# Performance work log

Hardware: AMD Instinct MI355X
Metric: run time of the kernel (lower is better)

## Reference

```python
import jax, jax.numpy as jnp
import numpy as np

C = 256

def setup_inputs() -> dict:
    key = jax.random.key(0)
    ks = jax.random.split(key, 7)
    s = 1.0 / np.sqrt(C)
    x = jax.random.normal(ks[0], (4, C, 64, 64), dtype=jnp.float32)
    Wq = jax.random.uniform(ks[1], (C, C), jnp.float32, -s, s)
    bq = jax.random.uniform(ks[2], (C,), jnp.float32, -s, s)
    Wk = jax.random.uniform(ks[3], (C, C), jnp.float32, -s, s)
    bk = jax.random.uniform(ks[4], (C,), jnp.float32, -s, s)
    Wv = jax.random.uniform(ks[5], (C, C), jnp.float32, -s, s)
    bv = jax.random.uniform(ks[6], (C,), jnp.float32, -s, s)
    return {"x": x, "Wq": Wq, "bq": bq, "Wk": Wk, "bk": bk, "Wv": Wv, "bv": bv}

def reference(x, Wq, bq, Wk, bk, Wv, bv):
    B, Cc, H, W = x.shape
    N = H * W
    xf = x.reshape(B, Cc, N)                      # (B, C, N)
    # 1x1 conv == channel linear: out[b,o,n] = sum_c W[o,c] x[b,c,n] + b[o]
    q = jnp.einsum('oc,bcn->bno', Wq, xf) + bq    # (B, N, C)  proj_query^T
    k = jnp.einsum('oc,bcn->bon', Wk, xf) + bk[None, :, None]  # (B, C, N)
    v = jnp.einsum('oc,bcn->bon', Wv, xf) + bv[None, :, None]  # (B, C, N)
    energy = jnp.einsum('bnc,bcm->bnm', q, k)     # (B, N, N)
    attention = jax.nn.softmax(energy, axis=-1)
    # out = V @ attention^T : out[b,c,n] = sum_m v[b,c,m] * attention[b,n,m]
    out = jnp.einsum('bcm,bnm->bcn', v, attention)
    return out.reshape(B, Cc, H, W)
```

## Files before the change

kernel.cpp:

```cpp
#include <hip/hip_runtime.h>
#include <math.h>

#define BB 4
#define CC 256
#define NN 4096

using half8 = __attribute__((ext_vector_type(8))) _Float16;
using f32x4 = __attribute__((ext_vector_type(4))) float;

__device__ __forceinline__ unsigned short f2h(float f) {
  _Float16 h = (_Float16)f;
  return __builtin_bit_cast(unsigned short, h);
}
__device__ __forceinline__ float h2f(unsigned short u) {
  return (float)__builtin_bit_cast(_Float16, u);
}

#define ASYNC16(g, l)                                                        \
  __builtin_amdgcn_global_load_lds(                                          \
      (const __attribute__((address_space(1))) unsigned int*)(g),            \
      (__attribute__((address_space(3))) unsigned int*)(l), 16, 0, 0)

__device__ __forceinline__ int row512_off(int r, int chunk) {
  return r * 256 + (((chunk & 24) | ((chunk ^ r) & 7)) << 3);
}
__device__ __forceinline__ int vt_off(int r, int chunk) {
  return r * 64 + (((chunk ^ r) & 7) << 3);
}

__global__ __launch_bounds__(256) void k_wcast(const float* __restrict__ Wq,
    const float* __restrict__ Wk, const float* __restrict__ Wv,
    unsigned short* __restrict__ Wt) {
  int id = blockIdx.x * 256 + threadIdx.x;
  int pos8 = id & 7, o = (id >> 3) & 255, ks = (id >> 11) & 3, p3 = id >> 13;
  const float* W = p3 == 0 ? Wq : (p3 == 1 ? Wk : Wv);
  int c = ks * 64 + ((pos8 ^ o) & 7) * 8;
  const float* src = W + (size_t)o * CC + c;
  float4 a = *(const float4*)(src);
  float4 b4 = *(const float4*)(src + 4);
  union { unsigned short u[8]; uint4 v4; } pk;
  pk.u[0] = f2h(a.x);  pk.u[1] = f2h(a.y);  pk.u[2] = f2h(a.z);  pk.u[3] = f2h(a.w);
  pk.u[4] = f2h(b4.x); pk.u[5] = f2h(b4.y); pk.u[6] = f2h(b4.z); pk.u[7] = f2h(b4.w);
  *(uint4*)(Wt + (size_t)id * 8) = pk.v4;
}

__global__ __launch_bounds__(512) void k_proj(const float* __restrict__ x,
    const unsigned short* __restrict__ Wt,
    const float* __restrict__ bq, const float* __restrict__ bk,
    const float* __restrict__ bv,
    unsigned short* __restrict__ Q, unsigned short* __restrict__ K,
    unsigned short* __restrict__ V) {
  __shared__ __align__(16) char ps[110848];
  float* xf = (float*)ps;
  unsigned short* xa = (unsigned short*)(ps + 8448);
  unsigned short* wh = (unsigned short*)(ps + 12544);
  int b = blockIdx.y, n0 = blockIdx.x * 32;
  int t = threadIdx.x, w = t >> 6, lane = t & 63, l15 = lane & 15, quad = lane >> 4;

  f32x4 z = {0.f, 0.f, 0.f, 0.f};
  f32x4 acc[3][2][2];
#pragma unroll
  for (int p3 = 0; p3 < 3; ++p3)
#pragma unroll
    for (int ct = 0; ct < 2; ++ct)
#pragma unroll
      for (int mt = 0; mt < 2; ++mt) acc[p3][ct][mt] = z;

  for (int ks = 0; ks < 4; ++ks) {
    if (ks) __syncthreads();
#pragma unroll
    for (int p3 = 0; p3 < 3; ++p3) {
      const char* wb = (const char*)(Wt + (size_t)(p3 * 4 + ks) * 16384);
#pragma unroll
      for (int p = 0; p < 4; ++p) {
        int c = p * 512 + t;
        ASYNC16(wb + c * 16, &wh[p3 * 16384 + (p * 512 + (w << 6)) * 8]);
      }
    }
    {
      int c = t >> 3, nl = (t & 7) * 4;
      float4 v = *(const float4*)(x + ((size_t)b * CC + ks * 64 + c) * NN + n0 + nl);
      float* d = xf + c * 33 + nl;
      d[0] = v.x; d[1] = v.y; d[2] = v.z; d[3] = v.w;
    }
    __syncthreads();
    {
      int n = t >> 4, cb = (t & 15) * 4;
      union { unsigned short u[4]; ushort4 v4; } tmp;
#pragma unroll
      for (int i = 0; i < 4; ++i) tmp.u[i] = f2h(xf[(cb + i) * 33 + n]);
      int ch = cb >> 3;
      *(ushort4*)&xa[n * 64 + (((ch ^ n) & 7) << 3) + (cb & 7)] = tmp.v4;
    }
    __syncthreads();
#pragma unroll
    for (int kc = 0; kc < 2; ++kc) {
      half8 af[2];
#pragma unroll
      for (int mt = 0; mt < 2; ++mt)
        af[mt] = *(const half8*)&xa[vt_off(mt * 16 + l15, kc * 4 + quad)];
#pragma unroll
      for (int p3 = 0; p3 < 3; ++p3)
#pragma unroll
        for (int ct = 0; ct < 2; ++ct) {
          half8 bf = *(const half8*)&wh[p3 * 16384 + vt_off(w * 32 + ct * 16 + l15, kc * 4 + quad)];
#pragma unroll
          for (int mt = 0; mt < 2; ++mt)
            acc[p3][ct][mt] = __builtin_amdgcn_mfma_f32_16x16x32_f16(af[mt], bf, acc[p3][ct][mt], 0, 0, 0);
        }
    }
  }
#pragma unroll
  for (int p3 = 0; p3 < 3; ++p3) {
    const float* bias = p3 == 0 ? bq : (p3 == 1 ? bk : bv);
#pragma unroll
    for (int ct = 0; ct < 2; ++ct) {
      float bv_ = bias[w * 32 + ct * 16 + l15];
#pragma unroll
      for (int mt = 0; mt < 2; ++mt)
#pragma unroll
        for (int r = 0; r < 4; ++r) acc[p3][ct][mt][r] += bv_;
    }
  }
#pragma unroll
  for (int p3 = 0; p3 < 2; ++p3) {
    __syncthreads();
    unsigned short* qo = (unsigned short*)ps;
#pragma unroll
    for (int ct = 0; ct < 2; ++ct)
#pragma unroll
      for (int mt = 0; mt < 2; ++mt)
#pragma unroll
        for (int r = 0; r < 4; ++r)
          qo[(mt * 16 + quad * 4 + r) * 264 + w * 32 + ct * 16 + l15] = f2h(acc[p3][ct][mt][r]);
    __syncthreads();
    unsigned short* outp = (p3 == 0 ? Q : K) + ((size_t)b * NN + n0) * CC;
#pragma unroll
    for (int p = 0; p < 2; ++p) {
      int f = p * 8192 + t * 16;
      int n = f >> 9, off = f & 511;
      *(uint4*)((char*)outp + (size_t)n * 512 + off) =
        *(const uint4*)((const char*)&qo[n * 264] + off);
    }
  }
  {
    __syncthreads();
    unsigned short* vo = (unsigned short*)ps;
#pragma unroll
    for (int ct = 0; ct < 2; ++ct)
#pragma unroll
      for (int mt = 0; mt < 2; ++mt)
#pragma unroll
        for (int r = 0; r < 4; ++r)
          vo[(w * 32 + ct * 16 + l15) * 36 + mt * 16 + quad * 4 + r] = f2h(acc[2][ct][mt][r]);
    __syncthreads();
#pragma unroll
    for (int p = 0; p < 2; ++p) {
      int id = p * 512 + t;
      int o = id >> 2, off = (id & 3) * 16;
      *(uint4*)((char*)(V + ((size_t)b * CC + o) * NN + n0) + off) =
        *(const uint4*)((const char*)&vo[o * 36] + off);
    }
  }
}

__global__ __launch_bounds__(512) void k_flash(const unsigned short* __restrict__ Q,
    const unsigned short* __restrict__ K, const unsigned short* __restrict__ V,
    float* __restrict__ out, unsigned short* __restrict__ opart,
    float* __restrict__ ml, int n_splits) {
  __shared__ unsigned short ktA[16384], ktB[16384];
  __shared__ unsigned short vt[16384];
  __shared__ unsigned short pt[8192];
  __shared__ float al[128], ll[128];
  int b = blockIdx.y, q0 = blockIdx.x * 128, split = blockIdx.z;
  int nper = 64 / n_splits;
  int t = threadIdx.x, w = t >> 6, lane = t & 63, l15 = lane & 15, quad = lane >> 4;
  int g = w >> 1, h = w & 1;

  half8 qf[8];
  const unsigned short* qrow = Q + ((size_t)b * NN + q0 + w * 16 + l15) * CC;
#pragma unroll
  for (int k = 0; k < 8; ++k) qf[k] = *(const half8*)(qrow + k * 32 + quad * 8);

  f32x4 z = {0.f, 0.f, 0.f, 0.f};
  f32x4 o_acc[2][8];
#pragma unroll
  for (int mt = 0; mt < 2; ++mt)
#pragma unroll
    for (int i = 0; i < 8; ++i) o_acc[mt][i] = z;
  float m_i[4], lp_[4];
#pragma unroll
  for (int r = 0; r < 4; ++r) { m_i[r] = -INFINITY; lp_[r] = 0.f; }

  int it_beg = split * nper, it_end = it_beg + nper;

  auto dma_k = [&](int it, unsigned short* dst) {
    const char* kb = (const char*)(K + ((size_t)b * NN + it * 64) * CC);
#pragma unroll
    for (int p = 0; p < 4; ++p) {
      int c = p * 512 + t;
      int r = c >> 5, lo = c & 31;
      int ch = (lo & 24) | ((lo ^ r) & 7);
      ASYNC16(kb + r * 512 + ch * 16, &dst[(p * 512 + (w << 6)) * 8]);
    }
  };
  auto dma_v = [&](int it) {
    const char* vb = (const char*)(V + (size_t)b * CC * NN + it * 64);
#pragma unroll
    for (int p = 0; p < 4; ++p) {
      int c = p * 512 + t;
      int r = c >> 3;
      int ch = (c ^ r) & 7;
      ASYNC16(vb + (size_t)r * 8192 + ch * 16, &vt[(p * 512 + (w << 6)) * 8]);
    }
  };

  auto body = [&](const unsigned short* cur, unsigned short* nxt, int it) {
    if (it + 1 < it_end) dma_k(it + 1, nxt);
    dma_v(it);

    f32x4 sa[4];
#pragma unroll
    for (int j = 0; j < 4; ++j) sa[j] = z;
#pragma unroll
    for (int kk = 0; kk < 8; ++kk) {
#pragma unroll
      for (int j = 0; j < 4; ++j) {
        half8 bf = *(const half8*)&cur[row512_off(j * 16 + l15, kk * 4 + quad)];
        sa[j] = __builtin_amdgcn_mfma_f32_16x16x32_f16(qf[kk], bf, sa[j], 0, 0, 0);
      }
    }
    float mt4[4];
#pragma unroll
    for (int r = 0; r < 4; ++r)
      mt4[r] = fmaxf(fmaxf(sa[0][r], sa[1][r]), fmaxf(sa[2][r], sa[3][r]));
#pragma unroll
    for (int off = 1; off < 16; off <<= 1)
#pragma unroll
      for (int r = 0; r < 4; ++r)
        mt4[r] = fmaxf(mt4[r], __shfl_xor(mt4[r], off, 64));
    float alpha[4];
#pragma unroll
    for (int r = 0; r < 4; ++r) {
      float mn = fmaxf(m_i[r], mt4[r]);
      alpha[r] = __expf(m_i[r] - mn);
      m_i[r] = mn;
    }
#pragma unroll
    for (int r = 0; r < 4; ++r) {
      float ls = 0.f;
#pragma unroll
      for (int j = 0; j < 4; ++j) {
        float p = __expf(sa[j][r] - m_i[r]);
        sa[j][r] = p;
        ls += p;
      }
      lp_[r] = lp_[r] * alpha[r] + ls;
    }
    if (l15 == 0) {
#pragma unroll
      for (int r = 0; r < 4; ++r) al[w * 16 + quad * 4 + r] = alpha[r];
    }
#pragma unroll
    for (int j = 0; j < 4; ++j)
#pragma unroll
      for (int r = 0; r < 4; ++r) {
        int row = w * 16 + quad * 4 + r;
        int ch = 2 * j + (l15 >> 3);
        pt[row * 64 + (((ch ^ row) & 7) << 3) + (l15 & 7)] = f2h(sa[j][r]);
      }
    __syncthreads();

    float a_al[2][4];
#pragma unroll
    for (int mt = 0; mt < 2; ++mt)
#pragma unroll
      for (int r = 0; r < 4; ++r)
        a_al[mt][r] = al[g * 32 + mt * 16 + quad * 4 + r];
#pragma unroll
    for (int mt = 0; mt < 2; ++mt)
#pragma unroll
      for (int ct = 0; ct < 8; ++ct)
#pragma unroll
        for (int r = 0; r < 4; ++r) o_acc[mt][ct][r] *= a_al[mt][r];
#pragma unroll
    for (int ks2 = 0; ks2 < 2; ++ks2) {
      half8 af[2];
#pragma unroll
      for (int mt = 0; mt < 2; ++mt) {
        int row_p = g * 32 + mt * 16 + l15;
        af[mt] = *(const half8*)&pt[row_p * 64 + ((((ks2 * 4 + quad) ^ row_p) & 7) << 3)];
      }
#pragma unroll
      for (int ct = 0; ct < 8; ++ct) {
        half8 bf = *(const half8*)&vt[vt_off(h * 128 + ct * 16 + l15, ks2 * 4 + quad)];
#pragma unroll
        for (int mt = 0; mt < 2; ++mt)
          o_acc[mt][ct] = __builtin_amdgcn_mfma_f32_16x16x32_f16(af[mt], bf, o_acc[mt][ct], 0, 0, 0);
      }
    }
    __syncthreads();
  };

  dma_k(it_beg, ktA);
  __syncthreads();
  for (int it = it_beg; it < it_end; it += 2) {
    body(ktA, ktB, it);
    body(ktB, ktA, it + 1);
  }

#pragma unroll
  for (int off = 1; off < 16; off <<= 1)
#pragma unroll
    for (int r = 0; r < 4; ++r)
      lp_[r] += __shfl_xor(lp_[r], off, 64);
  if (l15 == 0) {
#pragma unroll
    for (int r = 0; r < 4; ++r) ll[w * 16 + quad * 4 + r] = lp_[r];
  }
  if (n_splits != 1 && l15 == 0) {
    size_t qi = (size_t)q0 + w * 16 + quad * 4;
    float* mp = ml + ((size_t)(split * 2 + 0) * BB + b) * NN + qi;
    float* lq = ml + ((size_t)(split * 2 + 1) * BB + b) * NN + qi;
#pragma unroll
    for (int r = 0; r < 4; ++r) { mp[r] = m_i[r]; lq[r] = lp_[r]; }
  }
  __syncthreads();
  float sc[2][4];
#pragma unroll
  for (int mt = 0; mt < 2; ++mt)
#pragma unroll
    for (int r = 0; r < 4; ++r) {
      float lv = ll[g * 32 + mt * 16 + quad * 4 + r];
      sc[mt][r] = (n_splits == 1) ? 1.f / lv : 1.f;
    }

  float* od = (float*)ktA;
  float* obf = out + (size_t)b * CC * NN + q0;
  unsigned short* obh = opart + ((size_t)split * BB + b) * CC * NN + q0;
#pragma unroll
  for (int pp = 0; pp < 8; ++pp) {
    __syncthreads();
    if (h == (pp >> 2)) {
#pragma unroll
      for (int cp = 0; cp < 2; ++cp) {
        int ct = (pp & 3) * 2 + cp;
#pragma unroll
        for (int mt = 0; mt < 2; ++mt)
#pragma unroll
          for (int r = 0; r < 4; ++r)
            od[(cp * 16 + l15) * 132 + g * 32 + mt * 16 + quad * 4 + r] =
                o_acc[mt][ct][r] * sc[mt][r];
      }
    }
    __syncthreads();
    if (n_splits == 1) {
#pragma unroll
      for (int p2 = 0; p2 < 2; ++p2) {
        int row = p2 * 16 + (t >> 5);
        *(float4*)(obf + (size_t)(pp * 32 + row) * NN + (t & 31) * 4) =
          *(const float4*)&od[row * 132 + (t & 31) * 4];
      }
    } else {
      int row = t >> 4, q8 = (t & 15) * 8;
      union { unsigned short u[8]; uint4 v4; } tmp;
#pragma unroll
      for (int i2 = 0; i2 < 8; ++i2) tmp.u[i2] = f2h(od[row * 132 + q8 + i2]);
      *(uint4*)(obh + (size_t)(pp * 32 + row) * NN + q8) = tmp.v4;
    }
  }
}

__global__ __launch_bounds__(256) void k_merge(const unsigned short* __restrict__ opart,
    const float* __restrict__ ml, float* __restrict__ out) {
  size_t i = ((size_t)blockIdx.x * 256 + threadIdx.x) * 4;
  int n = (int)(i & (NN - 1));
  int b = (int)(i >> 20);
  float4 m1 = *(const float4*)(ml + ((size_t)(0 * BB) + b) * NN + n);
  float4 l1 = *(const float4*)(ml + ((size_t)(1 * BB) + b) * NN + n);
  float4 m2 = *(const float4*)(ml + ((size_t)(2 * BB) + b) * NN + n);
  float4 l2 = *(const float4*)(ml + ((size_t)(3 * BB) + b) * NN + n);
  ushort4 o1 = *(const ushort4*)(opart + i);
  ushort4 o2 = *(const ushort4*)(opart + (size_t)BB * CC * NN + i);
  float4 res;
#define MRG(f, comp) { \
    float M = fmaxf(m1.f, m2.f); \
    float e1 = __expf(m1.f - M), e2 = __expf(m2.f - M); \
    res.f = (e1 * h2f(o1.comp) + e2 * h2f(o2.comp)) / (e1 * l1.f + e2 * l2.f); }
  MRG(x, x) MRG(y, y) MRG(z, z) MRG(w, w)
#undef MRG
  *(float4*)(out + i) = res;
}

extern "C" void kernel_launch(void* const* d_in, const int* in_sizes, int n_in,
                              void* d_out, int out_size, void* d_ws, size_t ws_size,
                              hipStream_t stream) {
  const float* x  = (const float*)d_in[0];
  const float* Wq = (const float*)d_in[1];
  const float* bq = (const float*)d_in[2];
  const float* Wk = (const float*)d_in[3];
  const float* bk = (const float*)d_in[4];
  const float* Wv = (const float*)d_in[5];
  const float* bv = (const float*)d_in[6];
  float* out = (float*)d_out;
  char* ws = (char*)d_ws;
  const size_t MB = 1024 * 1024;
  unsigned short* Qb = (unsigned short*)(ws);
  unsigned short* Kb = (unsigned short*)(ws + 8 * MB);
  unsigned short* Vb = (unsigned short*)(ws + 16 * MB);
  unsigned short* Op = (unsigned short*)(ws + 24 * MB);
  float*          Ml = (float*)(ws + 40 * MB);

  int ns = (ws_size >= 41 * MB) ? 2 : 1;
  unsigned short* Wt = (unsigned short*)(ns == 2 ? ws + 40 * MB + 256 * 1024
                                                 : ws + 24 * MB);

  k_wcast<<<dim3(96), 256, 0, stream>>>(Wq, Wk, Wv, Wt);
  k_proj<<<dim3(128, 4), 512, 0, stream>>>(x, Wt, bq, bk, bv, Qb, Kb, Vb);

  k_flash<<<dim3(32, 4, ns), 512, 0, stream>>>(Qb, Kb, Vb, out, Op, Ml, ns);
  if (ns == 2) k_merge<<<dim3(4096), 256, 0, stream>>>(Op, Ml, out);
}
```

Baseline: 212.0 us.

## Halve flash KV tile to 32, raise occupancy, add 4-way split merge

```diff
diff --git a/kernel.cpp b/kernel.cpp
--- a/kernel.cpp
+++ b/kernel.cpp
@@ -4,6 +4,7 @@
 #define BB 4
 #define CC 256
 #define NN 4096
+#define KV 32
 
 using half8 = __attribute__((ext_vector_type(8))) _Float16;
 using f32x4 = __attribute__((ext_vector_type(4))) float;
@@ -23,6 +24,9 @@
 
 __device__ __forceinline__ int row512_off(int r, int chunk) {
   return r * 256 + (((chunk & 24) | ((chunk ^ r) & 7)) << 3);
+}
+__device__ __forceinline__ int tile32_off(int r, int q) {
+  return (r >> 1) * 64 + (((((r & 1) << 2) | q) ^ ((r >> 1) & 7)) & 7) * 8;
 }
 __device__ __forceinline__ int vt_off(int r, int chunk) {
   return r * 64 + (((chunk ^ r) & 7) << 3);
@@ -164,16 +168,19 @@
   }
 }
 
-__global__ __launch_bounds__(512) void k_flash(const unsigned short* __restrict__ Q,
+__global__ __launch_bounds__(512, 4) void k_flash(const unsigned short* __restrict__ Q,
     const unsigned short* __restrict__ K, const unsigned short* __restrict__ V,
     float* __restrict__ out, unsigned short* __restrict__ opart,
     float* __restrict__ ml, int n_splits) {
-  __shared__ unsigned short ktA[16384], ktB[16384];
-  __shared__ unsigned short vt[16384];
-  __shared__ unsigned short pt[8192];
-  __shared__ float al[128], ll[128];
+  __shared__ __align__(16) char sm[58368];
+  unsigned short* kt0 = (unsigned short*)sm;
+  unsigned short* kt1 = (unsigned short*)(sm + 16384);
+  unsigned short* vt  = (unsigned short*)(sm + 32768);
+  unsigned short* pt  = (unsigned short*)(sm + 49152);
+  float* al = (float*)(sm + 57344);
+  float* ll = (float*)(sm + 57856);
   int b = blockIdx.y, q0 = blockIdx.x * 128, split = blockIdx.z;
-  int nper = 64 / n_splits;
+  int nt = (NN / KV) / n_splits;
   int t = threadIdx.x, w = t >> 6, lane = t & 63, l15 = lane & 15, quad = lane >> 4;
   int g = w >> 1, h = w & 1;
 
@@ -192,12 +199,12 @@
 #pragma unroll
   for (int r = 0; r < 4; ++r) { m_i[r] = -INFINITY; lp_[r] = 0.f; }
 
-  int it_beg = split * nper, it_end = it_beg + nper;
+  int it_beg = split * nt, it_end = it_beg + nt;
 
   auto dma_k = [&](int it, unsigned short* dst) {
-    const char* kb = (const char*)(K + ((size_t)b * NN + it * 64) * CC);
-#pragma unroll
-    for (int p = 0; p < 4; ++p) {
+    const char* kb = (const char*)(K + ((size_t)b * NN + it * KV) * CC);
+#pragma unroll
+    for (int p = 0; p < 2; ++p) {
       int c = p * 512 + t;
       int r = c >> 5, lo = c & 31;
       int ch = (lo & 24) | ((lo ^ r) & 7);
@@ -205,13 +212,14 @@
     }
   };
   auto dma_v = [&](int it) {
-    const char* vb = (const char*)(V + (size_t)b * CC * NN + it * 64);
-#pragma unroll
-    for (int p = 0; p < 4; ++p) {
-      int c = p * 512 + t;
-      int r = c >> 3;
-      int ch = (c ^ r) & 7;
-      ASYNC16(vb + (size_t)r * 8192 + ch * 16, &vt[(p * 512 + (w << 6)) * 8]);
+    const char* vb = (const char*)(V + (size_t)b * CC * NN + it * KV);
+#pragma unroll
+    for (int p = 0; p < 2; ++p) {
+      int id = p * 512 + t;
+      int unit = id >> 3, u = id & 7;
+      int x = u ^ (unit & 7);
+      int r = unit * 2 + (x >> 2), ch = x & 3;
+      ASYNC16(vb + (size_t)r * (NN * 2) + ch * 16, &vt[(p * 512 + (w << 6)) * 8]);
     }
   };
 
@@ -219,21 +227,21 @@
     if (it + 1 < it_end) dma_k(it + 1, nxt);
     dma_v(it);
 
-    f32x4 sa[4];
-#pragma unroll
-    for (int j = 0; j < 4; ++j) sa[j] = z;
-#pragma unroll
-    for (int kk = 0; kk < 8; ++kk) {
-#pragma unroll
-      for (int j = 0; j < 4; ++j) {
+    f32x4 sa[2];
+#pragma unroll
+    for (int j = 0; j < 2; ++j) sa[j] = z;
+    __builtin_amdgcn_s_setprio(1);
+#pragma unroll
+    for (int kk = 0; kk < 8; ++kk)
+#pragma unroll
+      for (int j = 0; j < 2; ++j) {
         half8 bf = *(const half8*)&cur[row512_off(j * 16 + l15, kk * 4 + quad)];
         sa[j] = __builtin_amdgcn_mfma_f32_16x16x32_f16(qf[kk], bf, sa[j], 0, 0, 0);
       }
-    }
+    __builtin_amdgcn_s_setprio(0);
     float mt4[4];
 #pragma unroll
-    for (int r = 0; r < 4; ++r)
-      mt4[r] = fmaxf(fmaxf(sa[0][r], sa[1][r]), fmaxf(sa[2][r], sa[3][r]));
+    for (int r = 0; r < 4; ++r) mt4[r] = fmaxf(sa[0][r], sa[1][r]);
 #pragma unroll
     for (int off = 1; off < 16; off <<= 1)
 #pragma unroll
@@ -250,7 +258,7 @@
     for (int r = 0; r < 4; ++r) {
       float ls = 0.f;
 #pragma unroll
-      for (int j = 0; j < 4; ++j) {
+      for (int j = 0; j < 2; ++j) {
         float p = __expf(sa[j][r] - m_i[r]);
         sa[j][r] = p;
         ls += p;
@@ -262,12 +270,12 @@
       for (int r = 0; r < 4; ++r) al[w * 16 + quad * 4 + r] = alpha[r];
     }
 #pragma unroll
-    for (int j = 0; j < 4; ++j)
+    for (int j = 0; j < 2; ++j)
 #pragma unroll
       for (int r = 0; r < 4; ++r) {
         int row = w * 16 + quad * 4 + r;
         int ch = 2 * j + (l15 >> 3);
-        pt[row * 64 + (((ch ^ row) & 7) << 3) + (l15 & 7)] = f2h(sa[j][r]);
+        pt[tile32_off(row, ch) + (l15 & 7)] = f2h(sa[j][r]);
       }
     __syncthreads();
 
@@ -283,30 +291,27 @@
       for (int ct = 0; ct < 8; ++ct)
 #pragma unroll
         for (int r = 0; r < 4; ++r) o_acc[mt][ct][r] *= a_al[mt][r];
-#pragma unroll
-    for (int ks2 = 0; ks2 < 2; ++ks2) {
-      half8 af[2];
-#pragma unroll
-      for (int mt = 0; mt < 2; ++mt) {
-        int row_p = g * 32 + mt * 16 + l15;
-        af[mt] = *(const half8*)&pt[row_p * 64 + ((((ks2 * 4 + quad) ^ row_p) & 7) << 3)];
-      }
-#pragma unroll
-      for (int ct = 0; ct < 8; ++ct) {
-        half8 bf = *(const half8*)&vt[vt_off(h * 128 + ct * 16 + l15, ks2 * 4 + quad)];
-#pragma unroll
-        for (int mt = 0; mt < 2; ++mt)
-          o_acc[mt][ct] = __builtin_amdgcn_mfma_f32_16x16x32_f16(af[mt], bf, o_acc[mt][ct], 0, 0, 0);
-      }
-    }
+    half8 af[2];
+#pragma unroll
+    for (int mt = 0; mt < 2; ++mt)
+      af[mt] = *(const half8*)&pt[tile32_off(g * 32 + mt * 16 + l15, quad)];
+    __builtin_amdgcn_s_setprio(1);
+#pragma unroll
+    for (int ct = 0; ct < 8; ++ct) {
+      half8 bf = *(const half8*)&vt[tile32_off(h * 128 + ct * 16 + l15, quad)];
+#pragma unroll
+      for (int mt = 0; mt < 2; ++mt)
+        o_acc[mt][ct] = __builtin_amdgcn_mfma_f32_16x16x32_f16(af[mt], bf, o_acc[mt][ct], 0, 0, 0);
+    }
+    __builtin_amdgcn_s_setprio(0);
     __syncthreads();
   };
 
-  dma_k(it_beg, ktA);
+  dma_k(it_beg, kt0);
   __syncthreads();
   for (int it = it_beg; it < it_end; it += 2) {
-    body(ktA, ktB, it);
-    body(ktB, ktA, it + 1);
+    body(kt0, kt1, it);
+    body(kt1, kt0, it + 1);
   }
 
 #pragma unroll
@@ -335,7 +340,7 @@
       sc[mt][r] = (n_splits == 1) ? 1.f / lv : 1.f;
     }
 
-  float* od = (float*)ktA;
+  float* od = (float*)sm;
   float* obf = out + (size_t)b * CC * NN + q0;
   unsigned short* obh = opart + ((size_t)split * BB + b) * CC * NN + q0;
 #pragma unroll
@@ -371,22 +376,29 @@
   }
 }
 
+template <int NS>
 __global__ __launch_bounds__(256) void k_merge(const unsigned short* __restrict__ opart,
     const float* __restrict__ ml, float* __restrict__ out) {
   size_t i = ((size_t)blockIdx.x * 256 + threadIdx.x) * 4;
   int n = (int)(i & (NN - 1));
   int b = (int)(i >> 20);
-  float4 m1 = *(const float4*)(ml + ((size_t)(0 * BB) + b) * NN + n);
-  float4 l1 = *(const float4*)(ml + ((size_t)(1 * BB) + b) * NN + n);
-  float4 m2 = *(const float4*)(ml + ((size_t)(2 * BB) + b) * NN + n);
-  float4 l2 = *(const float4*)(ml + ((size_t)(3 * BB) + b) * NN + n);
-  ushort4 o1 = *(const ushort4*)(opart + i);
-  ushort4 o2 = *(const ushort4*)(opart + (size_t)BB * CC * NN + i);
+  float4 m[NS], l[NS];
+  ushort4 o[NS];
+#pragma unroll
+  for (int s = 0; s < NS; ++s) {
+    m[s] = *(const float4*)(ml + ((size_t)(s * 2 + 0) * BB + b) * NN + n);
+    l[s] = *(const float4*)(ml + ((size_t)(s * 2 + 1) * BB + b) * NN + n);
+    o[s] = *(const ushort4*)(opart + (size_t)s * BB * CC * NN + i);
+  }
   float4 res;
 #define MRG(f, comp) { \
-    float M = fmaxf(m1.f, m2.f); \
-    float e1 = __expf(m1.f - M), e2 = __expf(m2.f - M); \
-    res.f = (e1 * h2f(o1.comp) + e2 * h2f(o2.comp)) / (e1 * l1.f + e2 * l2.f); }
+    float M = m[0].f; \
+    _Pragma("unroll") for (int s = 1; s < NS; ++s) M = fmaxf(M, m[s].f); \
+    float num = 0.f, den = 0.f; \
+    _Pragma("unroll") for (int s = 0; s < NS; ++s) { \
+      float e = __expf(m[s].f - M); \
+      num += e * h2f(o[s].comp); den += e * l[s].f; } \
+    res.f = num / den; }
   MRG(x, x) MRG(y, y) MRG(z, z) MRG(w, w)
 #undef MRG
   *(float4*)(out + i) = res;
@@ -409,15 +421,25 @@
   unsigned short* Kb = (unsigned short*)(ws + 8 * MB);
   unsigned short* Vb = (unsigned short*)(ws + 16 * MB);
   unsigned short* Op = (unsigned short*)(ws + 24 * MB);
-  float*          Ml = (float*)(ws + 40 * MB);
-
-  int ns = (ws_size >= 41 * MB) ? 2 : 1;
-  unsigned short* Wt = (unsigned short*)(ns == 2 ? ws + 40 * MB + 256 * 1024
-                                                 : ws + 24 * MB);
+
+  int ns = (ws_size >= 57 * MB) ? 4 : (ws_size >= 41 * MB ? 2 : 1);
+  float* Ml;
+  unsigned short* Wt;
+  if (ns == 4) {
+    Ml = (float*)(ws + 56 * MB);
+    Wt = (unsigned short*)(ws + 56 * MB + 512 * 1024);
+  } else if (ns == 2) {
+    Ml = (float*)(ws + 40 * MB);
+    Wt = (unsigned short*)(ws + 40 * MB + 256 * 1024);
+  } else {
+    Ml = (float*)(ws + 24 * MB);
+    Wt = (unsigned short*)(ws + 24 * MB);
+  }
 
   k_wcast<<<dim3(96), 256, 0, stream>>>(Wq, Wk, Wv, Wt);
   k_proj<<<dim3(128, 4), 512, 0, stream>>>(x, Wt, bq, bk, bv, Qb, Kb, Vb);
 
   k_flash<<<dim3(32, 4, ns), 512, 0, stream>>>(Qb, Kb, Vb, out, Op, Ml, ns);
-  if (ns == 2) k_merge<<<dim3(4096), 256, 0, stream>>>(Op, Ml, out);
-}
+  if (ns == 4)      k_merge<4><<<dim3(4096), 256, 0, stream>>>(Op, Ml, out);
+  else if (ns == 2) k_merge<2><<<dim3(4096), 256, 0, stream>>>(Op, Ml, out);
+}
```

After: 459.0 us. 117% more time.

## Software-pipeline flash attention: overlap QK of tile i with PV of tile i-1

Applied to the files above, without the earlier changes.

```diff
diff --git a/kernel.cpp b/kernel.cpp
--- a/kernel.cpp
+++ b/kernel.cpp
@@ -4,6 +4,7 @@
 #define BB 4
 #define CC 256
 #define NN 4096
+#define KV 32
 
 using half8 = __attribute__((ext_vector_type(8))) _Float16;
 using f32x4 = __attribute__((ext_vector_type(4))) float;
@@ -23,6 +24,9 @@
 
 __device__ __forceinline__ int row512_off(int r, int chunk) {
   return r * 256 + (((chunk & 24) | ((chunk ^ r) & 7)) << 3);
+}
+__device__ __forceinline__ int tile32_off(int r, int q) {
+  return (r >> 1) * 64 + (((((r & 1) << 2) | q) ^ ((r >> 1) & 7)) & 7) * 8;
 }
 __device__ __forceinline__ int vt_off(int r, int chunk) {
   return r * 64 + (((chunk ^ r) & 7) << 3);
@@ -168,12 +172,18 @@
     const unsigned short* __restrict__ K, const unsigned short* __restrict__ V,
     float* __restrict__ out, unsigned short* __restrict__ opart,
     float* __restrict__ ml, int n_splits) {
-  __shared__ unsigned short ktA[16384], ktB[16384];
-  __shared__ unsigned short vt[16384];
-  __shared__ unsigned short pt[8192];
-  __shared__ float al[128], ll[128];
+  __shared__ __align__(16) char sm[83456];
+  unsigned short* kt0 = (unsigned short*)sm;
+  unsigned short* kt1 = (unsigned short*)(sm + 16384);
+  unsigned short* vt0 = (unsigned short*)(sm + 32768);
+  unsigned short* vt1 = (unsigned short*)(sm + 49152);
+  unsigned short* pt0 = (unsigned short*)(sm + 65536);
+  unsigned short* pt1 = (unsigned short*)(sm + 73728);
+  float* al0 = (float*)(sm + 81920);
+  float* al1 = (float*)(sm + 82432);
+  float* ll  = (float*)(sm + 82944);
   int b = blockIdx.y, q0 = blockIdx.x * 128, split = blockIdx.z;
-  int nper = 64 / n_splits;
+  int nt = (NN / KV) / n_splits;
   int t = threadIdx.x, w = t >> 6, lane = t & 63, l15 = lane & 15, quad = lane >> 4;
   int g = w >> 1, h = w & 1;
 
@@ -192,48 +202,96 @@
 #pragma unroll
   for (int r = 0; r < 4; ++r) { m_i[r] = -INFINITY; lp_[r] = 0.f; }
 
-  int it_beg = split * nper, it_end = it_beg + nper;
+  int it_beg = split * nt, it_end = it_beg + nt;
 
   auto dma_k = [&](int it, unsigned short* dst) {
-    const char* kb = (const char*)(K + ((size_t)b * NN + it * 64) * CC);
-#pragma unroll
-    for (int p = 0; p < 4; ++p) {
+    const char* kb = (const char*)(K + ((size_t)b * NN + it * KV) * CC);
+#pragma unroll
+    for (int p = 0; p < 2; ++p) {
       int c = p * 512 + t;
       int r = c >> 5, lo = c & 31;
       int ch = (lo & 24) | ((lo ^ r) & 7);
       ASYNC16(kb + r * 512 + ch * 16, &dst[(p * 512 + (w << 6)) * 8]);
     }
   };
-  auto dma_v = [&](int it) {
-    const char* vb = (const char*)(V + (size_t)b * CC * NN + it * 64);
-#pragma unroll
-    for (int p = 0; p < 4; ++p) {
-      int c = p * 512 + t;
-      int r = c >> 3;
-      int ch = (c ^ r) & 7;
-      ASYNC16(vb + (size_t)r * 8192 + ch * 16, &vt[(p * 512 + (w << 6)) * 8]);
+  auto dma_v = [&](int it, unsigned short* dst) {
+    const char* vb = (const char*)(V + (size_t)b * CC * NN + it * KV);
+#pragma unroll
+    for (int p = 0; p < 2; ++p) {
+      int id = p * 512 + t;
+      int unit = id >> 3, u = id & 7;
+      int x2 = u ^ (unit & 7);
+      int r = unit * 2 + (x2 >> 2), ch = x2 & 3;
+      ASYNC16(vb + (size_t)r * (NN * 2) + ch * 16, &dst[(p * 512 + (w << 6)) * 8]);
     }
   };
 
-  auto body = [&](const unsigned short* cur, unsigned short* nxt, int it) {
-    if (it + 1 < it_end) dma_k(it + 1, nxt);
-    dma_v(it);
-
-    f32x4 sa[4];
-#pragma unroll
-    for (int j = 0; j < 4; ++j) sa[j] = z;
-#pragma unroll
-    for (int kk = 0; kk < 8; ++kk) {
-#pragma unroll
-      for (int j = 0; j < 4; ++j) {
-        half8 bf = *(const half8*)&cur[row512_off(j * 16 + l15, kk * 4 + quad)];
+  auto pv_step = [&](const unsigned short* pprev, const unsigned short* vprev,
+                     const float* alp) {
+    f32x4 aa[2];
+    aa[0] = *(const f32x4*)&alp[g * 32 + quad * 4];
+    aa[1] = *(const f32x4*)&alp[g * 32 + 16 + quad * 4];
+    int need = 0;
+#pragma unroll
+    for (int mt = 0; mt < 2; ++mt)
+#pragma unroll
+      for (int r = 0; r < 4; ++r) need |= (aa[mt][r] != 1.f);
+    if (__any(need)) {
+#pragma unroll
+      for (int mt = 0; mt < 2; ++mt)
+#pragma unroll
+        for (int ct = 0; ct < 8; ++ct)
+#pragma unroll
+          for (int r = 0; r < 4; ++r) o_acc[mt][ct][r] *= aa[mt][r];
+    }
+    half8 af[2];
+#pragma unroll
+    for (int mt = 0; mt < 2; ++mt)
+      af[mt] = *(const half8*)&pprev[tile32_off(g * 32 + mt * 16 + l15, quad)];
+    __builtin_amdgcn_s_setprio(1);
+#pragma unroll
+    for (int ct = 0; ct < 8; ++ct) {
+      half8 bf = *(const half8*)&vprev[tile32_off(h * 128 + ct * 16 + l15, quad)];
+#pragma unroll
+      for (int mt = 0; mt < 2; ++mt)
+        o_acc[mt][ct] = __builtin_amdgcn_mfma_f32_16x16x32_f16(af[mt], bf, o_acc[mt][ct], 0, 0, 0);
+    }
+    __builtin_amdgcn_s_setprio(0);
+  };
+
+  dma_k(it_beg, (it_beg & 1) ? kt1 : kt0);
+
+  for (int it = it_beg; it < it_end; ++it) {
+    int par = it & 1;
+    const unsigned short* kcur = par ? kt1 : kt0;
+    unsigned short* knxt       = par ? kt0 : kt1;
+    unsigned short* vcur       = par ? vt1 : vt0;
+    const unsigned short* vprev = par ? vt0 : vt1;
+    unsigned short* pcur       = par ? pt1 : pt0;
+    const unsigned short* pprev = par ? pt0 : pt1;
+    float* alc       = par ? al1 : al0;
+    const float* alp = par ? al0 : al1;
+
+    __syncthreads();
+
+    if (it + 1 < it_end) dma_k(it + 1, knxt);
+    dma_v(it, vcur);
+
+    f32x4 sa[2];
+    sa[0] = z; sa[1] = z;
+    __builtin_amdgcn_s_setprio(1);
+#pragma unroll
+    for (int kk = 0; kk < 8; ++kk)
+#pragma unroll
+      for (int j = 0; j < 2; ++j) {
+        half8 bf = *(const half8*)&kcur[row512_off(j * 16 + l15, kk * 4 + quad)];
         sa[j] = __builtin_amdgcn_mfma_f32_16x16x32_f16(qf[kk], bf, sa[j], 0, 0, 0);
       }
-    }
+    __builtin_amdgcn_s_setprio(0);
+
     float mt4[4];
 #pragma unroll
-    for (int r = 0; r < 4; ++r)
-      mt4[r] = fmaxf(fmaxf(sa[0][r], sa[1][r]), fmaxf(sa[2][r], sa[3][r]));
+    for (int r = 0; r < 4; ++r) mt4[r] = fmaxf(sa[0][r], sa[1][r]);
 #pragma unroll
     for (int off = 1; off < 16; off <<= 1)
 #pragma unroll
@@ -250,7 +308,7 @@
     for (int r = 0; r < 4; ++r) {
       float ls = 0.f;
 #pragma unroll
-      for (int j = 0; j < 4; ++j) {
+      for (int j = 0; j < 2; ++j) {
         float p = __expf(sa[j][r] - m_i[r]);
         sa[j][r] = p;
         ls += p;
@@ -258,55 +316,25 @@
       lp_[r] = lp_[r] * alpha[r] + ls;
     }
     if (l15 == 0) {
-#pragma unroll
-      for (int r = 0; r < 4; ++r) al[w * 16 + quad * 4 + r] = alpha[r];
-    }
-#pragma unroll
-    for (int j = 0; j < 4; ++j)
+      f32x4 a4 = {alpha[0], alpha[1], alpha[2], alpha[3]};
+      *(f32x4*)&alc[w * 16 + quad * 4] = a4;
+    }
+#pragma unroll
+    for (int j = 0; j < 2; ++j)
 #pragma unroll
       for (int r = 0; r < 4; ++r) {
         int row = w * 16 + quad * 4 + r;
         int ch = 2 * j + (l15 >> 3);
-        pt[row * 64 + (((ch ^ row) & 7) << 3) + (l15 & 7)] = f2h(sa[j][r]);
-      }
-    __syncthreads();
-
-    float a_al[2][4];
-#pragma unroll
-    for (int mt = 0; mt < 2; ++mt)
-#pragma unroll
-      for (int r = 0; r < 4; ++r)
-        a_al[mt][r] = al[g * 32 + mt * 16 + quad * 4 + r];
-#pragma unroll
-    for (int mt = 0; mt < 2; ++mt)
-#pragma unroll
-      for (int ct = 0; ct < 8; ++ct)
-#pragma unroll
-        for (int r = 0; r < 4; ++r) o_acc[mt][ct][r] *= a_al[mt][r];
-#pragma unroll
-    for (int ks2 = 0; ks2 < 2; ++ks2) {
-      half8 af[2];
-#pragma unroll
-      for (int mt = 0; mt < 2; ++mt) {
-        int row_p = g * 32 + mt * 16 + l15;
-        af[mt] = *(const half8*)&pt[row_p * 64 + ((((ks2 * 4 + quad) ^ row_p) & 7) << 3)];
-      }
-#pragma unroll
-      for (int ct = 0; ct < 8; ++ct) {
-        half8 bf = *(const half8*)&vt[vt_off(h * 128 + ct * 16 + l15, ks2 * 4 + quad)];
-#pragma unroll
-        for (int mt = 0; mt < 2; ++mt)
-          o_acc[mt][ct] = __builtin_amdgcn_mfma_f32_16x16x32_f16(af[mt], bf, o_acc[mt][ct], 0, 0, 0);
-      }
-    }
-    __syncthreads();
-  };
-
-  dma_k(it_beg, ktA);
-  __syncthreads();
-  for (int it = it_beg; it < it_end; it += 2) {
-    body(ktA, ktB, it);
-    body(ktB, ktA, it + 1);
+        pcur[tile32_off(row, ch) + (l15 & 7)] = f2h(sa[j][r]);
+      }
+
+    if (it > it_beg) pv_step(pprev, vprev, alp);
+  }
+
+  {
+    int par = (it_end - 1) & 1;
+    __syncthreads();
+    pv_step(par ? pt1 : pt0, par ? vt1 : vt0, par ? al1 : al0);
   }
 
 #pragma unroll
@@ -335,7 +363,7 @@
       sc[mt][r] = (n_splits == 1) ? 1.f / lv : 1.f;
     }
 
-  float* od = (float*)ktA;
+  float* od = (float*)sm;
   float* obf = out + (size_t)b * CC * NN + q0;
   unsigned short* obh = opart + ((size_t)split * BB + b) * CC * NN + q0;
 #pragma unroll
```

Result: slower. 234.0 us (+10.4%).
